# Performance work log

Hardware: AMD Instinct MI355X
Metric: run time of the kernel (lower is better)

Reference implementation:

```python
import jax, jax.numpy as jnp
import numpy as np

N_NODES = 50000


def _degree_norms(edge_index, n_nodes):
    # PyG GCNConv: add self-loops, deg = 1 + in-degree at target (col)
    src, dst = edge_index[0], edge_index[1]
    deg = 1.0 + jax.ops.segment_sum(jnp.ones(src.shape[0], jnp.float32), dst,
                                    num_segments=n_nodes)
    d_inv_sqrt = 1.0 / jnp.sqrt(deg)  # deg >= 1 always (self-loop)
    norm_e = d_inv_sqrt[src] * d_inv_sqrt[dst]   # per-edge sym norm
    norm_self = d_inv_sqrt * d_inv_sqrt          # self-loop weight
    return norm_e, norm_self


def _gcn_conv(x, W, b, src, dst, norm_e, norm_self, n_nodes):
    h = x @ W                                    # [N, F_out]
    msg = h[src] * norm_e[:, None]               # gather + scale, [E, F_out]
    agg = jax.ops.segment_sum(msg, dst, num_segments=n_nodes)
    return agg + norm_self[:, None] * h + b


def setup_inputs() -> dict:
    key = jax.random.key(0)
    ks = jax.random.split(key, 10)
    F_in, H = 128, 128
    E = 1_600_000
    x = jax.random.normal(ks[0], (N_NODES, F_in), jnp.float32)
    edge_index = jax.random.randint(ks[1], (2, E), 0, N_NODES, dtype=jnp.int64)

    def glorot(k, fi, fo):
        s = jnp.sqrt(6.0 / (fi + fo)).astype(jnp.float32)
        return jax.random.uniform(k, (fi, fo), jnp.float32, -s, s)

    return {
        "x": x,
        "edge_index": edge_index,
        "W1": glorot(ks[2], F_in, H), "b1": jnp.zeros((H,), jnp.float32),
        "W2": glorot(ks[3], H, H),    "b2": jnp.zeros((H,), jnp.float32),
        "W3": glorot(ks[4], H, H),    "b3": jnp.zeros((H,), jnp.float32),
        "W4": glorot(ks[5], H, 1),    "b4": jnp.zeros((1,), jnp.float32),
    }


def reference(x, edge_index, W1, b1, W2, b2, W3, b3, W4, b4):
    src, dst = edge_index[0], edge_index[1]
    norm_e, norm_self = _degree_norms(edge_index, N_NODES)
    h = jax.nn.relu(_gcn_conv(x, W1, b1, src, dst, norm_e, norm_self, N_NODES))
    h = jax.nn.relu(_gcn_conv(h, W2, b2, src, dst, norm_e, norm_self, N_NODES))
    h = jax.nn.relu(_gcn_conv(h, W3, b3, src, dst, norm_e, norm_self, N_NODES))
    return _gcn_conv(h, W4, b4, src, dst, norm_e, norm_self, N_NODES)
```

## Files before the change

kernel.cpp:

```cpp
#include <hip/hip_runtime.h>
#include <hip/hip_bf16.h>
#include <stdint.h>

typedef unsigned int u32;
typedef unsigned short u16;

#define F 128

typedef __attribute__((ext_vector_type(8))) short bf16x8;
typedef __attribute__((ext_vector_type(4))) float f32x4;

__device__ __forceinline__ float bf2f(u16 v){
  union { u32 u; float f; } x; x.u = ((u32)v) << 16; return x.f;
}
__device__ __forceinline__ u16 f2bf(float f){
  union { float f; u32 u; } x; x.f = f;
  u32 u = x.u;
  return (u16)((u + 0x7fffu + ((u >> 16) & 1u)) >> 16);
}

__global__ void k_dtype(const u32* __restrict__ w, int nwords, int* __restrict__ isf32){
  u32 hit = 0;
  for (int i = threadIdx.x; i < nwords; i += blockDim.x){
    u32 e = (w[i] >> 7) & 0xFFu;
    if (e > 160u) hit = 1;
  }
  if (hit) atomicOr(isf32, 1);
}

__global__ void k_detect(const u32* __restrict__ w, int ncheck, int* __restrict__ flag){
  u32 v = 0;
  for (int i = threadIdx.x; i < ncheck; i += blockDim.x) v |= w[2*i + 1];
  if (v) atomicOr(flag, 1);
}

__launch_bounds__(256)
__global__ void k_bhist(const u32* __restrict__ w, int E, const int* __restrict__ flagp,
                        int NB, int* __restrict__ bcnt){
  __shared__ int h[256];
  int st = (*flagp) ? 1 : 2;
  int t = threadIdx.x;
  h[t] = 0;
  __syncthreads();
  int base = blockIdx.x*4096;
  #pragma unroll 4
  for (int k = 0; k < 16; k++){
    int i = base + k*256 + t;
    if (i < E){
      int d = (int)w[(size_t)(E + i)*st];
      atomicAdd(&h[d >> 8], 1);
    }
  }
  __syncthreads();
  if (t < NB && h[t]) atomicAdd(&bcnt[t], h[t]);
}

__global__ void k_bscan(const int* __restrict__ bcnt, int NB, int E,
                        int* __restrict__ bbase, int* __restrict__ bump){
  __shared__ int s[256];
  int t = threadIdx.x;
  int v = (t < NB) ? bcnt[t] : 0;
  s[t] = v;
  __syncthreads();
  for (int off = 1; off < 256; off <<= 1){
    int x = (t >= off) ? s[t - off] : 0;
    __syncthreads();
    s[t] += x;
    __syncthreads();
  }
  bbase[t] = s[t] - v;
  if (t == 255) bbase[256] = E;
  bump[t] = 0;
}

__launch_bounds__(256)
__global__ void k_msplit(const u32* __restrict__ w, int E, const int* __restrict__ flagp,
                         const int* __restrict__ bbase, int* __restrict__ bump,
                         u32* __restrict__ ebuf){
  __shared__ int h[256];
  __shared__ int cb[256];
  int st = (*flagp) ? 1 : 2;
  int t = threadIdx.x;
  h[t] = 0;
  __syncthreads();
  int base = blockIdx.x*4096;
  u32 ps[16]; int bk[16]; int rk[16];
  #pragma unroll 4
  for (int k = 0; k < 16; k++){
    int i = base + k*256 + t;
    if (i < E){
      u32 s = w[(size_t)i*st];
      u32 d = w[(size_t)(E + i)*st];
      bk[k] = (int)(d >> 8);
      ps[k] = (s & 0xFFFFu) | ((d & 0xFFu) << 16);
      rk[k] = atomicAdd(&h[bk[k]], 1);
    } else bk[k] = -1;
  }
  __syncthreads();
  cb[t] = h[t] ? (bbase[t] + atomicAdd(&bump[t], h[t])) : 0;
  __syncthreads();
  #pragma unroll 4
  for (int k = 0; k < 16; k++){
    if (bk[k] >= 0) ebuf[cb[bk[k]] + rk[k]] = ps[k];
  }
}

__launch_bounds__(256)
__global__ void k_bemit(const u32* __restrict__ ebuf, const int* __restrict__ bbase,
                        int N, int* __restrict__ deg, int* __restrict__ rs,
                        u16* __restrict__ csr){
  __shared__ int nd[256];
  __shared__ int nofs[256];
  __shared__ int s[256];
  int b = blockIdx.x;
  int t = threadIdx.x;
  int e0 = bbase[b], e1 = bbase[b + 1];
  nd[t] = 0;
  __syncthreads();
  for (int i = e0 + t; i < e1; i += 256) atomicAdd(&nd[ebuf[i] >> 16], 1);
  __syncthreads();
  int v = nd[t];
  s[t] = v;
  __syncthreads();
  for (int off = 1; off < 256; off <<= 1){
    int x = (t >= off) ? s[t - off] : 0;
    __syncthreads();
    s[t] += x;
    __syncthreads();
  }
  nofs[t] = s[t] - v;
  int node = b*256 + t;
  if (node < N){ deg[node] = v; rs[node] = e0 + nofs[t]; }
  nd[t] = 0;
  __syncthreads();
  for (int i = e0 + t; i < e1; i += 256){
    u32 p = ebuf[i];
    int d = (int)(p >> 16);
    int pos = e0 + nofs[d] + atomicAdd(&nd[d], 1);
    csr[pos] = (u16)(p & 0xFFFFu);
  }
}

__global__ void k_dis(const int* __restrict__ deg, float* __restrict__ dis, int N){
  int i = blockIdx.x*blockDim.x + threadIdx.x;
  if (i < N) dis[i] = rsqrtf(1.0f + (float)deg[i]);
}

__global__ void k_cvt_f(const void* __restrict__ in, const int* __restrict__ isf32,
                        float* __restrict__ out, int n){
  int i = blockIdx.x*blockDim.x + threadIdx.x;
  if (i < n){
    out[i] = (*isf32) ? ((const float*)in)[i] : bf2f(((const u16*)in)[i]);
  }
}

__global__ void k_cvt_b(const void* __restrict__ in, const int* __restrict__ isf32,
                        u16* __restrict__ out, int n){
  int i = blockIdx.x*blockDim.x + threadIdx.x;
  if (i < n){
    float v = (*isf32) ? ((const float*)in)[i] : bf2f(((const u16*)in)[i]);
    out[i] = f2bf(v);
  }
}

__global__ void k_swz(const void* __restrict__ W, const int* __restrict__ isf32,
                      u16* __restrict__ WL){
  int idx = blockIdx.x*256 + threadIdx.x;
  int j    = idx & 7;
  int lane = (idx >> 3) & 63;
  int kb   = (idx >> 9) & 3;
  int ct   = idx >> 11;
  int m = lane & 15, q = lane >> 4;
  int k = kb*32 + q*8 + j;
  int c = ct*16 + m;
  float v = (*isf32) ? ((const float*)W)[k*F + c] : bf2f(((const u16*)W)[k*F + c]);
  WL[idx] = f2bf(v);
}

__launch_bounds__(256)
__global__ void k_mm(const u16* __restrict__ X, const u16* __restrict__ WL,
                     const float* __restrict__ dis, u16* __restrict__ G, int N){
  int w = threadIdx.x >> 6, lane = threadIdx.x & 63;
  int m = lane & 15, q = lane >> 4;
  int row0 = blockIdx.x*64 + w*16;
  int arow = row0 + m;
  bf16x8 a[4];
  if (arow < N){
    const u16* xp = X + (size_t)arow*F;
    #pragma unroll
    for (int kb = 0; kb < 4; kb++) a[kb] = *(const bf16x8*)(xp + kb*32 + q*8);
  } else {
    #pragma unroll
    for (int kb = 0; kb < 4; kb++) a[kb] = (bf16x8){0,0,0,0,0,0,0,0};
  }
  f32x4 acc[8];
  #pragma unroll
  for (int ct = 0; ct < 8; ct++) acc[ct] = (f32x4){0.f,0.f,0.f,0.f};
  #pragma unroll
  for (int ct = 0; ct < 8; ct++){
    #pragma unroll
    for (int kb = 0; kb < 4; kb++){
      bf16x8 b = *(const bf16x8*)(WL + ((size_t)((ct*4 + kb)*64 + lane))*8);
      acc[ct] = __builtin_amdgcn_mfma_f32_16x16x32_bf16(a[kb], b, acc[ct], 0, 0, 0);
    }
  }
  int rbase = row0 + q*4;
  #pragma unroll
  for (int r = 0; r < 4; r++){
    int row = rbase + r;
    if (row < N){
      float dv = dis[row];
      #pragma unroll
      for (int ct = 0; ct < 8; ct++)
        G[(size_t)row*F + ct*16 + m] = f2bf(dv*acc[ct][r]);
    }
  }
}

__launch_bounds__(256)
__global__ void k_agg(const u16* __restrict__ G, const float* __restrict__ dis,
                      const int* __restrict__ rs, const int* __restrict__ deg,
                      const u16* __restrict__ csr, const float* __restrict__ bias,
                      u16* __restrict__ Xout, int N, int relu){
  int wid  = blockIdx.x*4 + (threadIdx.x >> 6);
  int lane = threadIdx.x & 63;
  if (wid >= N) return;
  int base = rs[wid], len = deg[wid];
  u32 sw = *(const u32*)(G + (size_t)wid*F + 2*lane);
  float a0 = bf2f((u16)sw), a1 = bf2f((u16)(sw >> 16));
  float p0=0.f,p1=0.f,p2=0.f,p3=0.f,q0=0.f,q1=0.f,q2=0.f,q3=0.f;
  for (int c0 = 0; c0 < len; c0 += 64){
    int mm = len - c0; if (mm > 64) mm = 64;
    int sidx = (lane < mm) ? (int)csr[base + c0 + lane] : 0;
    int j = 0;
    for (; j + 4 <= mm; j += 4){
      int s0 = __builtin_amdgcn_readlane(sidx, j);
      int s1 = __builtin_amdgcn_readlane(sidx, j+1);
      int s2 = __builtin_amdgcn_readlane(sidx, j+2);
      int s3 = __builtin_amdgcn_readlane(sidx, j+3);
      u32 w0 = *(const u32*)(G + (size_t)s0*F + 2*lane);
      u32 w1 = *(const u32*)(G + (size_t)s1*F + 2*lane);
      u32 w2 = *(const u32*)(G + (size_t)s2*F + 2*lane);
      u32 w3 = *(const u32*)(G + (size_t)s3*F + 2*lane);
      p0 += bf2f((u16)w0); q0 += bf2f((u16)(w0 >> 16));
      p1 += bf2f((u16)w1); q1 += bf2f((u16)(w1 >> 16));
      p2 += bf2f((u16)w2); q2 += bf2f((u16)(w2 >> 16));
      p3 += bf2f((u16)w3); q3 += bf2f((u16)(w3 >> 16));
    }
    for (; j < mm; j++){
      int s0 = __builtin_amdgcn_readlane(sidx, j);
      u32 w0 = *(const u32*)(G + (size_t)s0*F + 2*lane);
      p0 += bf2f((u16)w0); q0 += bf2f((u16)(w0 >> 16));
    }
  }
  a0 += (p0 + p1) + (p2 + p3);
  a1 += (q0 + q1) + (q2 + q3);
  float dv = dis[wid];
  float o0 = fmaf(dv, a0, bias[2*lane]);
  float o1 = fmaf(dv, a1, bias[2*lane + 1]);
  if (relu){ o0 = fmaxf(o0, 0.f); o1 = fmaxf(o1, 0.f); }
  *(u32*)(Xout + (size_t)wid*F + 2*lane) = (u32)f2bf(o0) | ((u32)f2bf(o1) << 16);
}

__global__ void k_mm4(const u16* __restrict__ X, const float* __restrict__ W4f,
                      const float* __restrict__ dis, float* __restrict__ G4, int N){
  int gt   = blockIdx.x*blockDim.x + threadIdx.x;
  int wid  = gt >> 6;
  int lane = threadIdx.x & 63;
  if (wid >= N) return;
  u32 xw = *(const u32*)(X + (size_t)wid*F + 2*lane);
  float acc = bf2f((u16)xw)*W4f[2*lane] + bf2f((u16)(xw >> 16))*W4f[2*lane + 1];
  #pragma unroll
  for (int off = 32; off > 0; off >>= 1) acc += __shfl_down(acc, off, 64);
  if (lane == 0) G4[wid] = dis[wid]*acc;
}

__global__ void k_agg4(const float* __restrict__ G4, const float* __restrict__ dis,
                       const int* __restrict__ rs, const int* __restrict__ deg,
                       const u16* __restrict__ csr, const float* __restrict__ b4f,
                       const int* __restrict__ isf32, void* __restrict__ out, int N){
  int i = blockIdx.x*blockDim.x + threadIdx.x;
  if (i >= N) return;
  int base = rs[i], len = deg[i];
  float acc = G4[i];
  for (int j = 0; j < len; j++) acc += G4[csr[base + j]];
  float r = dis[i]*acc + b4f[0];
  if (*isf32) ((float*)out)[i] = r;
  else        ((u16*)out)[i]   = f2bf(r);
}

extern "C" void kernel_launch(void* const* d_in, const int* in_sizes, int n_in,
                              void* d_out, int out_size, void* d_ws, size_t ws_size,
                              hipStream_t stream){
  const void* x0 = d_in[0];
  const u32*  ei = (const u32*)d_in[1];
  const void* Wp[4] = {d_in[2], d_in[4], d_in[6], d_in[8]};
  const void* bp[4] = {d_in[3], d_in[5], d_in[7], d_in[9]};
  int N = in_sizes[0] / F;
  int E = in_sizes[1] / 2;
  int NB = (N + 255) >> 8;

  char* base = (char*)d_ws;
  size_t off = 0;
  auto alloc = [&](size_t bytes)->char*{
    char* p = base + off;
    off = (off + bytes + 255) & ~(size_t)255;
    return p;
  };
  int*   deg  = (int*)  alloc((size_t)N*4);
  float* dis  = (float*)alloc((size_t)N*4);
  int*   rs   = (int*)  alloc((size_t)N*4);
  float* g4   = (float*)alloc((size_t)N*4);
  int*   bcnt = (int*)  alloc(1024);
  int*   bbase= (int*)  alloc(1056);
  int*   bump = (int*)  alloc(1024);
  int*   flags= (int*)  alloc(256);
  u32*   ebuf = (u32*)  alloc((size_t)E*4);
  u16*   csr  = (u16*)  alloc((size_t)E*2);
  u16*   WL   = (u16*)  alloc(16384*2);
  float* wf4  = (float*)alloc(F*4);
  float* bb   = (float*)alloc(F*4);
  float* bb4  = (float*)alloc(256);
  u16*   gbuf = (u16*)  alloc((size_t)N*F*2);
  u16*   xbuf = (u16*)  alloc((size_t)N*F*2);

  hipMemsetAsync(bcnt, 0, 1024, stream);
  hipMemsetAsync(flags, 0, 256, stream);

  int* eflag = flags + 0;
  int* isf32 = flags + 1;

  int nbt = (N + 255)/256;
  int etb = (E + 4095)/4096;

  k_dtype <<<1, 256, 0, stream>>>((const u32*)x0, 2048, isf32);
  k_detect<<<1, 256, 0, stream>>>(ei, 4096, eflag);
  k_bhist <<<etb, 256, 0, stream>>>(ei, E, eflag, NB, bcnt);
  k_bscan <<<1, 256, 0, stream>>>(bcnt, NB, E, bbase, bump);
  k_msplit<<<etb, 256, 0, stream>>>(ei, E, eflag, bbase, bump, ebuf);
  k_bemit <<<NB, 256, 0, stream>>>(ebuf, bbase, N, deg, rs, csr);
  k_dis   <<<nbt, 256, 0, stream>>>(deg, dis, N);

  int mmb = (N + 63)/64;
  int agb = (N + 3)/4;

  k_cvt_b<<<((size_t)N*F + 255)/256, 256, 0, stream>>>(x0, isf32, xbuf, N*F);

  for (int l = 0; l < 3; l++){
    k_swz  <<<64, 256, 0, stream>>>(Wp[l], isf32, WL);
    k_cvt_f<<<1, 128, 0, stream>>>(bp[l], isf32, bb, F);
    k_mm   <<<mmb, 256, 0, stream>>>(xbuf, WL, dis, gbuf, N);
    k_agg  <<<agb, 256, 0, stream>>>(gbuf, dis, rs, deg, csr, bb, xbuf, N, 1);
  }
  k_cvt_f<<<1, 128, 0, stream>>>(Wp[3], isf32, wf4, F);
  k_cvt_f<<<1, 64, 0, stream>>>(bp[3], isf32, bb4, 1);
  k_mm4  <<<((size_t)N*64 + 255)/256, 256, 0, stream>>>(xbuf, wf4, dis, g4, N);
  k_agg4 <<<nbt, 256, 0, stream>>>(g4, dis, rs, deg, csr, bb4, isf32, (void*)d_out, N);
}
```

Before: 404.4 us.

## Store features in column-chunked layout and split aggregation per 32-feature chunk

```diff
diff --git a/kernel.cpp b/kernel.cpp
--- a/kernel.cpp
+++ b/kernel.cpp
@@ -19,19 +19,20 @@
   return (u16)((u + 0x7fffu + ((u >> 16) & 1u)) >> 16);
 }
 
-__global__ void k_dtype(const u32* __restrict__ w, int nwords, int* __restrict__ isf32){
-  u32 hit = 0;
-  for (int i = threadIdx.x; i < nwords; i += blockDim.x){
-    u32 e = (w[i] >> 7) & 0xFFu;
-    if (e > 160u) hit = 1;
-  }
-  if (hit) atomicOr(isf32, 1);
-}
-
-__global__ void k_detect(const u32* __restrict__ w, int ncheck, int* __restrict__ flag){
-  u32 v = 0;
-  for (int i = threadIdx.x; i < ncheck; i += blockDim.x) v |= w[2*i + 1];
-  if (v) atomicOr(flag, 1);
+__global__ void k_flags(const u32* __restrict__ xw, const u32* __restrict__ ei,
+                        int* __restrict__ flags){
+  if (blockIdx.x == 0){
+    u32 hit = 0;
+    for (int i = threadIdx.x; i < 2048; i += 256){
+      u32 e = (xw[i] >> 7) & 0xFFu;
+      if (e > 160u) hit = 1;
+    }
+    if (hit) atomicOr(&flags[1], 1);
+  } else {
+    u32 v = 0;
+    for (int i = threadIdx.x; i < 4096; i += 256) v |= ei[2*i + 1];
+    if (v) atomicOr(&flags[0], 1);
+  }
 }
 
 __launch_bounds__(256)
@@ -108,7 +109,7 @@
 __launch_bounds__(256)
 __global__ void k_bemit(const u32* __restrict__ ebuf, const int* __restrict__ bbase,
                         int N, int* __restrict__ deg, int* __restrict__ rs,
-                        u16* __restrict__ csr){
+                        u16* __restrict__ csr, float* __restrict__ dis){
   __shared__ int nd[256];
   __shared__ int nofs[256];
   __shared__ int s[256];
@@ -130,7 +131,11 @@
   }
   nofs[t] = s[t] - v;
   int node = b*256 + t;
-  if (node < N){ deg[node] = v; rs[node] = e0 + nofs[t]; }
+  if (node < N){
+    deg[node] = v;
+    rs[node]  = e0 + nofs[t];
+    dis[node] = rsqrtf(1.0f + (float)v);
+  }
   nd[t] = 0;
   __syncthreads();
   for (int i = e0 + t; i < e1; i += 256){
@@ -141,31 +146,40 @@
   }
 }
 
-__global__ void k_dis(const int* __restrict__ deg, float* __restrict__ dis, int N){
+__global__ void k_prep(const void* b1, const void* b2, const void* b3,
+                       const void* W4, const void* b4, const int* __restrict__ isf32,
+                       float* __restrict__ bb, float* __restrict__ wf4,
+                       float* __restrict__ bb4){
+  int t = threadIdx.x;
+  int f32 = *isf32;
+  if (t < 384){
+    const void* s = (t < 128) ? b1 : ((t < 256) ? b2 : b3);
+    int i = t & 127;
+    bb[t] = f32 ? ((const float*)s)[i] : bf2f(((const u16*)s)[i]);
+  } else if (t < 512){
+    int i = t - 384;
+    wf4[i] = f32 ? ((const float*)W4)[i] : bf2f(((const u16*)W4)[i]);
+  } else if (t == 512){
+    bb4[0] = f32 ? ((const float*)b4)[0] : bf2f(((const u16*)b4)[0]);
+  }
+}
+
+__global__ void k_cvt_b(const void* __restrict__ in, const int* __restrict__ isf32,
+                        u16* __restrict__ out, int N){
   int i = blockIdx.x*blockDim.x + threadIdx.x;
-  if (i < N) dis[i] = rsqrtf(1.0f + (float)deg[i]);
-}
-
-__global__ void k_cvt_f(const void* __restrict__ in, const int* __restrict__ isf32,
-                        float* __restrict__ out, int n){
-  int i = blockIdx.x*blockDim.x + threadIdx.x;
+  int n = N*F;
   if (i < n){
-    out[i] = (*isf32) ? ((const float*)in)[i] : bf2f(((const u16*)in)[i]);
-  }
-}
-
-__global__ void k_cvt_b(const void* __restrict__ in, const int* __restrict__ isf32,
-                        u16* __restrict__ out, int n){
-  int i = blockIdx.x*blockDim.x + threadIdx.x;
-  if (i < n){
+    int r = i >> 7, f = i & 127;
     float v = (*isf32) ? ((const float*)in)[i] : bf2f(((const u16*)in)[i]);
-    out[i] = f2bf(v);
-  }
-}
-
-__global__ void k_swz(const void* __restrict__ W, const int* __restrict__ isf32,
-                      u16* __restrict__ WL){
-  int idx = blockIdx.x*256 + threadIdx.x;
+    __builtin_nontemporal_store(f2bf(v), &out[((size_t)(f >> 5)*N + r)*32 + (f & 31)]);
+  }
+}
+
+__global__ void k_swz3(const void* W1, const void* W2, const void* W3,
+                       const int* __restrict__ isf32, u16* __restrict__ WL){
+  int l = blockIdx.x >> 6;
+  const void* W = (l == 0) ? W1 : ((l == 1) ? W2 : W3);
+  int idx = (blockIdx.x & 63)*256 + threadIdx.x;
   int j    = idx & 7;
   int lane = (idx >> 3) & 63;
   int kb   = (idx >> 9) & 3;
@@ -174,7 +188,7 @@
   int k = kb*32 + q*8 + j;
   int c = ct*16 + m;
   float v = (*isf32) ? ((const float*)W)[k*F + c] : bf2f(((const u16*)W)[k*F + c]);
-  WL[idx] = f2bf(v);
+  WL[l*16384 + idx] = f2bf(v);
 }
 
 __launch_bounds__(256)
@@ -186,9 +200,9 @@
   int arow = row0 + m;
   bf16x8 a[4];
   if (arow < N){
-    const u16* xp = X + (size_t)arow*F;
     #pragma unroll
-    for (int kb = 0; kb < 4; kb++) a[kb] = *(const bf16x8*)(xp + kb*32 + q*8);
+    for (int kb = 0; kb < 4; kb++)
+      a[kb] = *(const bf16x8*)(X + ((size_t)kb*N + arow)*32 + q*8);
   } else {
     #pragma unroll
     for (int kb = 0; kb < 4; kb++) a[kb] = (bf16x8){0,0,0,0,0,0,0,0};
@@ -211,8 +225,10 @@
     if (row < N){
       float dv = dis[row];
       #pragma unroll
-      for (int ct = 0; ct < 8; ct++)
-        G[(size_t)row*F + ct*16 + m] = f2bf(dv*acc[ct][r]);
+      for (int ct = 0; ct < 8; ct++){
+        __builtin_nontemporal_store(f2bf(dv*acc[ct][r]),
+            &G[((size_t)(ct >> 1)*N + row)*32 + (ct & 1)*16 + m]);
+      }
     }
   }
 }
@@ -222,44 +238,41 @@
                       const int* __restrict__ rs, const int* __restrict__ deg,
                       const u16* __restrict__ csr, const float* __restrict__ bias,
                       u16* __restrict__ Xout, int N, int relu){
-  int wid  = blockIdx.x*4 + (threadIdx.x >> 6);
+  int c    = (blockIdx.x & 7) >> 1;
+  int wid  = (blockIdx.x >> 3)*8 + (blockIdx.x & 1)*4 + (threadIdx.x >> 6);
   int lane = threadIdx.x & 63;
+  int slot = lane >> 4;
+  int fp   = lane & 15;
   if (wid >= N) return;
+  const u16* Gs = G + (size_t)c*N*32;
   int base = rs[wid], len = deg[wid];
-  u32 sw = *(const u32*)(G + (size_t)wid*F + 2*lane);
-  float a0 = bf2f((u16)sw), a1 = bf2f((u16)(sw >> 16));
   float p0=0.f,p1=0.f,p2=0.f,p3=0.f,q0=0.f,q1=0.f,q2=0.f,q3=0.f;
-  for (int c0 = 0; c0 < len; c0 += 64){
-    int mm = len - c0; if (mm > 64) mm = 64;
-    int sidx = (lane < mm) ? (int)csr[base + c0 + lane] : 0;
-    int j = 0;
-    for (; j + 4 <= mm; j += 4){
-      int s0 = __builtin_amdgcn_readlane(sidx, j);
-      int s1 = __builtin_amdgcn_readlane(sidx, j+1);
-      int s2 = __builtin_amdgcn_readlane(sidx, j+2);
-      int s3 = __builtin_amdgcn_readlane(sidx, j+3);
-      u32 w0 = *(const u32*)(G + (size_t)s0*F + 2*lane);
-      u32 w1 = *(const u32*)(G + (size_t)s1*F + 2*lane);
-      u32 w2 = *(const u32*)(G + (size_t)s2*F + 2*lane);
-      u32 w3 = *(const u32*)(G + (size_t)s3*F + 2*lane);
-      p0 += bf2f((u16)w0); q0 += bf2f((u16)(w0 >> 16));
-      p1 += bf2f((u16)w1); q1 += bf2f((u16)(w1 >> 16));
-      p2 += bf2f((u16)w2); q2 += bf2f((u16)(w2 >> 16));
-      p3 += bf2f((u16)w3); q3 += bf2f((u16)(w3 >> 16));
-    }
-    for (; j < mm; j++){
-      int s0 = __builtin_amdgcn_readlane(sidx, j);
-      u32 w0 = *(const u32*)(G + (size_t)s0*F + 2*lane);
-      p0 += bf2f((u16)w0); q0 += bf2f((u16)(w0 >> 16));
-    }
-  }
-  a0 += (p0 + p1) + (p2 + p3);
-  a1 += (q0 + q1) + (q2 + q3);
-  float dv = dis[wid];
-  float o0 = fmaf(dv, a0, bias[2*lane]);
-  float o1 = fmaf(dv, a1, bias[2*lane + 1]);
-  if (relu){ o0 = fmaxf(o0, 0.f); o1 = fmaxf(o1, 0.f); }
-  *(u32*)(Xout + (size_t)wid*F + 2*lane) = (u32)f2bf(o0) | ((u32)f2bf(o1) << 16);
+  for (int j = 0; j < len; j += 16){
+    int n0 = j + slot, n1 = j + 4 + slot, n2 = j + 8 + slot, n3 = j + 12 + slot;
+    u32 w0 = 0, w1 = 0, w2 = 0, w3 = 0;
+    if (n0 < len){ int s = csr[base + n0]; w0 = *(const u32*)(Gs + (size_t)s*32 + 2*fp); }
+    if (n1 < len){ int s = csr[base + n1]; w1 = *(const u32*)(Gs + (size_t)s*32 + 2*fp); }
+    if (n2 < len){ int s = csr[base + n2]; w2 = *(const u32*)(Gs + (size_t)s*32 + 2*fp); }
+    if (n3 < len){ int s = csr[base + n3]; w3 = *(const u32*)(Gs + (size_t)s*32 + 2*fp); }
+    p0 += bf2f((u16)w0); q0 += bf2f((u16)(w0 >> 16));
+    p1 += bf2f((u16)w1); q1 += bf2f((u16)(w1 >> 16));
+    p2 += bf2f((u16)w2); q2 += bf2f((u16)(w2 >> 16));
+    p3 += bf2f((u16)w3); q3 += bf2f((u16)(w3 >> 16));
+  }
+  float a0 = (p0 + p1) + (p2 + p3);
+  float a1 = (q0 + q1) + (q2 + q3);
+  a0 += __shfl_xor(a0, 16, 64); a0 += __shfl_xor(a0, 32, 64);
+  a1 += __shfl_xor(a1, 16, 64); a1 += __shfl_xor(a1, 32, 64);
+  if (slot == 0){
+    u32 sw = *(const u32*)(Gs + (size_t)wid*32 + 2*fp);
+    a0 += bf2f((u16)sw); a1 += bf2f((u16)(sw >> 16));
+    float dv = dis[wid];
+    float o0 = fmaf(dv, a0, bias[c*32 + 2*fp]);
+    float o1 = fmaf(dv, a1, bias[c*32 + 2*fp + 1]);
+    if (relu){ o0 = fmaxf(o0, 0.f); o1 = fmaxf(o1, 0.f); }
+    u32 pk = (u32)f2bf(o0) | ((u32)f2bf(o1) << 16);
+    __builtin_nontemporal_store(pk, (u32*)(Xout + ((size_t)c*N + wid)*32 + 2*fp));
+  }
 }
 
 __global__ void k_mm4(const u16* __restrict__ X, const float* __restrict__ W4f,
@@ -268,7 +281,7 @@
   int wid  = gt >> 6;
   int lane = threadIdx.x & 63;
   if (wid >= N) return;
-  u32 xw = *(const u32*)(X + (size_t)wid*F + 2*lane);
+  u32 xw = *(const u32*)(X + ((size_t)(lane >> 4)*N + wid)*32 + 2*(lane & 15));
   float acc = bf2f((u16)xw)*W4f[2*lane] + bf2f((u16)(xw >> 16))*W4f[2*lane + 1];
   #pragma unroll
   for (int off = 32; off > 0; off >>= 1) acc += __shfl_down(acc, off, 64);
@@ -282,9 +295,15 @@
   int i = blockIdx.x*blockDim.x + threadIdx.x;
   if (i >= N) return;
   int base = rs[i], len = deg[i];
-  float acc = G4[i];
-  for (int j = 0; j < len; j++) acc += G4[csr[base + j]];
-  float r = dis[i]*acc + b4f[0];
+  float a0 = 0.f, a1 = 0.f, a2 = 0.f, a3 = 0.f;
+  int j = 0;
+  for (; j + 4 <= len; j += 4){
+    int s0 = csr[base + j],     s1 = csr[base + j + 1];
+    int s2 = csr[base + j + 2], s3 = csr[base + j + 3];
+    a0 += G4[s0]; a1 += G4[s1]; a2 += G4[s2]; a3 += G4[s3];
+  }
+  for (; j < len; j++) a0 += G4[csr[base + j]];
+  float r = dis[i]*(G4[i] + ((a0 + a1) + (a2 + a3))) + b4f[0];
   if (*isf32) ((float*)out)[i] = r;
   else        ((u16*)out)[i]   = f2bf(r);
 }
@@ -317,9 +336,9 @@
   int*   flags= (int*)  alloc(256);
   u32*   ebuf = (u32*)  alloc((size_t)E*4);
   u16*   csr  = (u16*)  alloc((size_t)E*2);
-  u16*   WL   = (u16*)  alloc(16384*2);
+  u16*   WL   = (u16*)  alloc(3*16384*2);
   float* wf4  = (float*)alloc(F*4);
-  float* bb   = (float*)alloc(F*4);
+  float* bb   = (float*)alloc(3*F*4);
   float* bb4  = (float*)alloc(256);
   u16*   gbuf = (u16*)  alloc((size_t)N*F*2);
   u16*   xbuf = (u16*)  alloc((size_t)N*F*2);
@@ -333,27 +352,22 @@
   int nbt = (N + 255)/256;
   int etb = (E + 4095)/4096;
 
-  k_dtype <<<1, 256, 0, stream>>>((const u32*)x0, 2048, isf32);
-  k_detect<<<1, 256, 0, stream>>>(ei, 4096, eflag);
+  k_flags <<<2, 256, 0, stream>>>((const u32*)x0, ei, flags);
   k_bhist <<<etb, 256, 0, stream>>>(ei, E, eflag, NB, bcnt);
   k_bscan <<<1, 256, 0, stream>>>(bcnt, NB, E, bbase, bump);
   k_msplit<<<etb, 256, 0, stream>>>(ei, E, eflag, bbase, bump, ebuf);
-  k_bemit <<<NB, 256, 0, stream>>>(ebuf, bbase, N, deg, rs, csr);
-  k_dis   <<<nbt, 256, 0, stream>>>(deg, dis, N);
-
-  int mmb = (N + 63)/64;
-  int agb = (N + 3)/4;
-
-  k_cvt_b<<<((size_t)N*F + 255)/256, 256, 0, stream>>>(x0, isf32, xbuf, N*F);
+  k_bemit <<<NB, 256, 0, stream>>>(ebuf, bbase, N, deg, rs, csr, dis);
+  k_prep  <<<1, 640, 0, stream>>>(bp[0], bp[1], bp[2], Wp[3], bp[3], isf32, bb, wf4, bb4);
+  k_swz3  <<<192, 256, 0, stream>>>(Wp[0], Wp[1], Wp[2], isf32, WL);
+  k_cvt_b <<<((size_t)N*F + 255)/256, 256, 0, stream>>>(x0, isf32, xbuf, N);
+
+  int mmb  = (N + 63)/64;
+  int aggB = ((N + 7)/8)*8;
 
   for (int l = 0; l < 3; l++){
-    k_swz  <<<64, 256, 0, stream>>>(Wp[l], isf32, WL);
-    k_cvt_f<<<1, 128, 0, stream>>>(bp[l], isf32, bb, F);
-    k_mm   <<<mmb, 256, 0, stream>>>(xbuf, WL, dis, gbuf, N);
-    k_agg  <<<agb, 256, 0, stream>>>(gbuf, dis, rs, deg, csr, bb, xbuf, N, 1);
-  }
-  k_cvt_f<<<1, 128, 0, stream>>>(Wp[3], isf32, wf4, F);
-  k_cvt_f<<<1, 64, 0, stream>>>(bp[3], isf32, bb4, 1);
-  k_mm4  <<<((size_t)N*64 + 255)/256, 256, 0, stream>>>(xbuf, wf4, dis, g4, N);
-  k_agg4 <<<nbt, 256, 0, stream>>>(g4, dis, rs, deg, csr, bb4, isf32, (void*)d_out, N);
-}
+    k_mm <<<mmb, 256, 0, stream>>>(xbuf, WL + l*16384, dis, gbuf, N);
+    k_agg<<<aggB, 256, 0, stream>>>(gbuf, dis, rs, deg, csr, bb + l*F, xbuf, N, 1);
+  }
+  k_mm4 <<<((size_t)N*64 + 255)/256, 256, 0, stream>>>(xbuf, wf4, dis, g4, N);
+  k_agg4<<<nbt, 256, 0, stream>>>(g4, dis, rs, deg, csr, bb4, isf32, (void*)d_out, N);
+}
```

Measured after the change: 536.1 us. 32.6% more time.
